# Kernel tuning notes

Hardware: AMD Instinct MI355X
Metric: run time of the kernel (lower is better)

The kernel has to match this reference:

```python
import jax, jax.numpy as jnp
import numpy as np

EPS = 1e-06


def setup_inputs() -> dict:
    key = jax.random.key(0)
    k1, k2, k3 = jax.random.split(key, 3)
    B, L, S, C = 128, 512, 512, 64
    q = jax.random.normal(k1, (B, L, C), dtype=jnp.float32)
    k = jax.random.normal(k2, (B, S, C), dtype=jnp.float32)
    labels = jax.random.randint(k3, (B, L, S), 0, 2, dtype=jnp.int64)
    return {"q": q, "k": k, "labels": labels}


def reference(q, k, labels):
    # sim: [B, L, S], mapped to (0, 1) via (1 + cos-like sim) / 2
    sim = (1.0 + jnp.einsum('blc,bsc->bls', q, k)) * 0.5

    # column-wise stats (over L) -> [B, S]; torch.std uses ddof=1 (unbiased)
    col = (jnp.max(sim, axis=1) - jnp.mean(sim, axis=1)) / jnp.std(sim, axis=1, ddof=1)
    sharp1 = jax.nn.softmax(col, axis=-1)  # [B, S]

    # row-wise stats (over S) -> [B, L]
    row = (jnp.max(sim, axis=2) - jnp.mean(sim, axis=2)) / jnp.std(sim, axis=2, ddof=1)
    sharp2 = jax.nn.softmax(row, axis=-1)  # [B, L]

    simc = jnp.clip(sim, EPS, 1.0 - EPS)
    nll = -jnp.log(simc)                    # [B, L, S]
    nll_neg = -jnp.log(1.0 - simc)          # [B, L, S]

    pos = (labels == 1).astype(sim.dtype)
    neg = (labels == 0).astype(sim.dtype)

    # masked sums per sample, weighted by sharpness (broadcast over rows/cols)
    loss1 = jnp.sum(nll * sharp1[:, None, :] * pos, axis=(1, 2))  # [B]
    loss2 = jnp.sum(nll * sharp2[:, :, None] * pos, axis=(1, 2))  # [B]
    loss3 = jnp.sum(nll_neg * neg, axis=(1, 2)) / jnp.sum(neg, axis=(1, 2))  # [B]

    losses = (loss1 + loss2) * 0.5 + loss3
    return (sharp1, jnp.mean(losses))
```

## Files before the change

kernel.cpp:

```cpp
#include <hip/hip_runtime.h>

#define EPSF 1e-6f

typedef _Float16 half8 __attribute__((ext_vector_type(8)));
typedef float f32x4 __attribute__((ext_vector_type(4)));

constexpr int B = 128, L = 512, S = 512, C = 64;
constexpr int TILE_R = 64;
constexpr int TILES  = L / TILE_R;
constexpr int CHUNK  = 64;
constexpr int NCHUNK = S / CHUNK;
constexpr int HALVES = 2;
constexpr int CPB    = NCHUNK / HALVES;

constexpr size_t WS_COLMAX = 0;
constexpr size_t WS_COLSUM = WS_COLMAX + (size_t)B * TILES * S;
constexpr size_t WS_COLSSQ = WS_COLSUM + (size_t)B * TILES * S;
constexpr size_t WS_COLP1  = WS_COLSSQ + (size_t)B * TILES * S;
constexpr size_t WS_ROWMAX = WS_COLP1  + (size_t)B * TILES * S;
constexpr size_t WS_ROWSUM = WS_ROWMAX + (size_t)B * L * HALVES;
constexpr size_t WS_ROWSSQ = WS_ROWSUM + (size_t)B * L * HALVES;
constexpr size_t WS_ROWP2  = WS_ROWSSQ + (size_t)B * L * HALVES;
constexpr size_t WS_NEGS   = WS_ROWP2  + (size_t)B * L * HALVES;
constexpr size_t WS_NEGC   = WS_NEGS   + (size_t)B * TILES * HALVES;
constexpr size_t WS_QF     = WS_NEGC   + (size_t)B * TILES * HALVES;
constexpr size_t WS_KF     = WS_QF     + (size_t)B * TILES * 4096;
constexpr size_t WS_LP     = WS_KF     + (size_t)B * NCHUNK * 4096;

constexpr int PACK_ROWS   = 4;
constexpr int CONV_BLOCKS = B * (TILES + NCHUNK);
constexpr int PACK_BLOCKS = B * L / PACK_ROWS;

__device__ inline void loadTile(const float* __restrict__ g, float4 v[4], int t)
{
    const float* src = g + (t >> 2) * 64 + (t & 3) * 16;
    v[0] = *(const float4*)(src);
    v[1] = *(const float4*)(src + 4);
    v[2] = *(const float4*)(src + 8);
    v[3] = *(const float4*)(src + 12);
}

__device__ inline void fragStore(const float4 v4[4], half8* dhi, half8* dlo, int t)
{
    const int row = t >> 2, c0 = (t & 3) * 16;
    const float v[16] = {v4[0].x, v4[0].y, v4[0].z, v4[0].w, v4[1].x, v4[1].y, v4[1].z, v4[1].w,
                         v4[2].x, v4[2].y, v4[2].z, v4[2].w, v4[3].x, v4[3].y, v4[3].z, v4[3].w};
#pragma unroll
    for (int o = 0; o < 2; ++o) {
        const int cb     = c0 + o * 8;
        const int idx    = (row >> 4) * 2 + (cb >> 5);
        const int lane_s = (((cb >> 3) & 3) << 4) + (row & 15);
        half8 h, l;
#pragma unroll
        for (int j = 0; j < 8; ++j) {
            float f = v[o * 8 + j];
            _Float16 hi = (_Float16)f;
            h[j] = hi;
            l[j] = (_Float16)(f - (float)hi);
        }
        dhi[idx * 64 + lane_s] = h;
        dlo[idx * 64 + lane_s] = l;
    }
}

__global__ __launch_bounds__(256)
void convert_kernel(const float* __restrict__ q, const float* __restrict__ kmat,
                    const int* __restrict__ labels, float* __restrict__ ws)
{
    const int bidx = blockIdx.x;
    const int tid  = threadIdx.x;

    if (bidx < CONV_BLOCKS) {
        const int b    = bidx >> 4;
        const int t16  = bidx & 15;
        const bool isq = (t16 < TILES);
        const int tile = isq ? t16 : t16 - TILES;

        const float* src = isq ? (q    + ((size_t)b * L + (size_t)tile * TILE_R) * C)
                               : (kmat + ((size_t)b * S + (size_t)tile * CHUNK)  * C);
        half8* base = (half8*)(ws + (isq ? WS_QF : WS_KF)) + (size_t)(b * TILES + tile) * 1024;

        float4 v[4];
        loadTile(src, v, tid);
        fragStore(v, base, base + 512, tid);
    } else {
        const int pb   = bidx - CONV_BLOCKS;
        const int b    = pb / (L / PACK_ROWS);
        const int rg   = pb % (L / PACK_ROWS);
        const int wave = tid >> 6, lane = tid & 63;
        const size_t row = (size_t)b * L + rg * PACK_ROWS + wave;
        const int* src = labels + row * S;
        unsigned long long* dst = (unsigned long long*)(ws + WS_LP) + row * 8;
        int v[8];
#pragma unroll
        for (int w = 0; w < 8; ++w)
            v[w] = __builtin_nontemporal_load(&src[w * 64 + lane]);
#pragma unroll
        for (int w = 0; w < 8; ++w) {
            unsigned long long m = __ballot(v[w] == 1);
            if (lane == 0) dst[w] = m;
        }
    }
}

__device__ inline void gl16(const void* g, void* l)
{
    __builtin_amdgcn_global_load_lds((const __attribute__((address_space(1))) void*)g,
                                     (__attribute__((address_space(3))) void*)l, 16, 0, 0);
}

__global__ __launch_bounds__(256) __attribute__((amdgpu_waves_per_eu(3, 8)))
void pass1_kernel(float* __restrict__ ws)
{
    __shared__ half8 kbuf[2][1024];
    __shared__ float4 colred4[4][CPB][CHUNK];
    __shared__ float nred[4][2];

    const int bidx = blockIdx.x;
    const int b    = bidx / (TILES * HALVES);
    const int rem  = bidx % (TILES * HALVES);
    const int tile = rem >> 1;
    const int half = rem & 1;
    const int chbase = half * CPB;
    const int tid  = threadIdx.x;
    const int lane = tid & 63;
    const int wave = tid >> 6;
    const int l15  = lane & 15;
    const int quad = lane >> 4;
    const int rowbase = tile * TILE_R;

    float* colmax_p = ws + WS_COLMAX;
    float* colsum_p = ws + WS_COLSUM;
    float* colssq_p = ws + WS_COLSSQ;
    float* colp1_p  = ws + WS_COLP1;
    float* rowmax_p = ws + WS_ROWMAX;
    float* rowsum_p = ws + WS_ROWSUM;
    float* rowssq_p = ws + WS_ROWSSQ;
    float* rowp2_p  = ws + WS_ROWP2;
    float* negs_p   = ws + WS_NEGS;
    float* negc_p   = ws + WS_NEGC;

    const half8* qf  = (const half8*)(ws + WS_QF) + (size_t)(b * TILES + tile) * 1024;
    const half8* kf0 = (const half8*)(ws + WS_KF) + (size_t)b * NCHUNK * 1024;
    const unsigned long long* lp =
        (const unsigned long long*)(ws + WS_LP) + ((size_t)b * L + rowbase) * 8;

    auto stage = [&](int ch, int bi) {
#pragma unroll
        for (int i = 0; i < 4; ++i)
            gl16(kf0 + (size_t)ch * 1024 + i * 256 + tid,
                 &kbuf[bi][i * 256 + (tid & 192)]);
    };

    stage(chbase, 0);

    half8 ah0 = qf[(wave * 2 + 0) * 64 + lane];
    half8 ah1 = qf[(wave * 2 + 1) * 64 + lane];
    half8 al0 = qf[512 + (wave * 2 + 0) * 64 + lane];
    half8 al1 = qf[512 + (wave * 2 + 1) * 64 + lane];

    float rmax[4], rsum[4], rssq[4], rp2[4];
#pragma unroll
    for (int i = 0; i < 4; ++i) { rmax[i] = -3.4e38f; rsum[i] = 0.f; rssq[i] = 0.f; rp2[i] = 0.f; }
    float negsum = 0.f;
    int   possum = 0;

    __syncthreads();

    for (int c4 = 0; c4 < CPB; ++c4) {
        const int ch = chbase + c4;
        if (c4 + 1 < CPB) stage(ch + 1, (c4 + 1) & 1);
        const half8* kb = kbuf[c4 & 1];

        unsigned long long lw[4];
#pragma unroll
        for (int r = 0; r < 4; ++r)
            lw[r] = lp[(size_t)(wave * 16 + quad * 4 + r) * 8 + ch];

        f32x4 acc[4];
#pragma unroll
        for (int ct = 0; ct < 4; ++ct) {
            half8 bh0 = kb[(ct * 2 + 0) * 64 + lane];
            half8 bh1 = kb[(ct * 2 + 1) * 64 + lane];
            half8 bl0 = kb[512 + (ct * 2 + 0) * 64 + lane];
            half8 bl1 = kb[512 + (ct * 2 + 1) * 64 + lane];
            f32x4 a = {0.f, 0.f, 0.f, 0.f};
            a = __builtin_amdgcn_mfma_f32_16x16x32_f16(ah0, bh0, a, 0, 0, 0);
            a = __builtin_amdgcn_mfma_f32_16x16x32_f16(ah0, bl0, a, 0, 0, 0);
            a = __builtin_amdgcn_mfma_f32_16x16x32_f16(al0, bh0, a, 0, 0, 0);
            a = __builtin_amdgcn_mfma_f32_16x16x32_f16(ah1, bh1, a, 0, 0, 0);
            a = __builtin_amdgcn_mfma_f32_16x16x32_f16(ah1, bl1, a, 0, 0, 0);
            a = __builtin_amdgcn_mfma_f32_16x16x32_f16(al1, bh1, a, 0, 0, 0);
            acc[ct] = a;
        }

#pragma unroll
        for (int ct = 0; ct < 4; ++ct) {
            float cmax = -3.4e38f, csum = 0.f, cssq = 0.f, cp1 = 0.f;
#pragma unroll
            for (int r = 0; r < 4; ++r) {
                int lab = (int)((lw[r] >> (ct * 16 + l15)) & 1ull);
                float sim = fmaf(0.5f, acc[ct][r], 0.5f);
                rmax[r] = fmaxf(rmax[r], sim);
                rsum[r] += sim;
                rssq[r] = fmaf(sim, sim, rssq[r]);
                cmax = fmaxf(cmax, sim);
                csum += sim;
                cssq = fmaf(sim, sim, cssq);
                float sc  = fminf(fmaxf(sim, EPSF), 1.f - EPSF);
                bool  isp = (lab == 1);
                float pos = isp ? 1.f : 0.f;
                float t   = isp ? sc : (1.f - sc);
                float nl  = -__logf(t);
                float pn  = pos * nl;
                rp2[r] += pn;
                cp1 += pn;
                negsum += nl - pn;
                possum += lab;
            }
#pragma unroll
            for (int m = 16; m <= 32; m <<= 1) {
                cmax = fmaxf(cmax, __shfl_xor(cmax, m, 64));
                csum += __shfl_xor(csum, m, 64);
                cssq += __shfl_xor(cssq, m, 64);
                cp1  += __shfl_xor(cp1,  m, 64);
            }
            if (lane < 16)
                colred4[wave][c4][ct * 16 + l15] = make_float4(cmax, csum, cssq, cp1);
        }

        __syncthreads();
    }

    {
        const int cc  = tid >> 6;
        const int col = tid & 63;
        float4 v = colred4[0][cc][col];
        float m0 = v.x, s1 = v.y, s2 = v.z, pp = v.w;
#pragma unroll
        for (int w = 1; w < 4; ++w) {
            float4 u = colred4[w][cc][col];
            m0 = fmaxf(m0, u.x); s1 += u.y; s2 += u.z; pp += u.w;
        }
        size_t idx = ((size_t)b * TILES + tile) * S + (chbase + cc) * CHUNK + col;
        colmax_p[idx] = m0; colsum_p[idx] = s1; colssq_p[idx] = s2; colp1_p[idx] = pp;
    }

#pragma unroll
    for (int r = 0; r < 4; ++r) {
#pragma unroll
        for (int m = 1; m <= 8; m <<= 1) {
            rmax[r] = fmaxf(rmax[r], __shfl_xor(rmax[r], m, 64));
            rsum[r] += __shfl_xor(rsum[r], m, 64);
            rssq[r] += __shfl_xor(rssq[r], m, 64);
            rp2[r]  += __shfl_xor(rp2[r],  m, 64);
        }
    }
    if (l15 == 0) {
#pragma unroll
        for (int r = 0; r < 4; ++r) {
            size_t idx = ((size_t)b * L + rowbase + wave * 16 + quad * 4 + r) * HALVES + half;
            rowmax_p[idx] = rmax[r]; rowsum_p[idx] = rsum[r];
            rowssq_p[idx] = rssq[r]; rowp2_p[idx]  = rp2[r];
        }
    }

    float negcnt = (float)(16 * CPB - possum);
#pragma unroll
    for (int m = 1; m <= 32; m <<= 1) {
        negsum += __shfl_xor(negsum, m, 64);
        negcnt += __shfl_xor(negcnt, m, 64);
    }
    if (lane == 0) { nred[wave][0] = negsum; nred[wave][1] = negcnt; }
    __syncthreads();
    if (tid == 0) {
        float ns = 0.f, nc = 0.f;
        for (int w = 0; w < 4; ++w) { ns += nred[w][0]; nc += nred[w][1]; }
        negs_p[bidx] = ns; negc_p[bidx] = nc;
    }
}

template <bool MAX>
__device__ inline float bred(float v, float* red)
{
#pragma unroll
    for (int m = 1; m <= 32; m <<= 1) {
        float o = __shfl_xor(v, m, 64);
        v = MAX ? fmaxf(v, o) : (v + o);
    }
    const int wave = threadIdx.x >> 6;
    const int lane = threadIdx.x & 63;
    if (lane == 0) red[wave] = v;
    __syncthreads();
    if (threadIdx.x == 0) {
        float r = red[0];
        for (int w = 1; w < 8; ++w) r = MAX ? fmaxf(r, red[w]) : (r + red[w]);
        red[8] = r;
    }
    __syncthreads();
    float out = red[8];
    __syncthreads();
    return out;
}

__global__ __launch_bounds__(512)
void pass2_kernel(const float* __restrict__ ws, float* __restrict__ out)
{
    __shared__ float red[9];
    const int b = blockIdx.x;
    const int s = threadIdx.x;

    if (blockIdx.y == 0) {
        const float* colmax_p = ws + WS_COLMAX;
        const float* colsum_p = ws + WS_COLSUM;
        const float* colssq_p = ws + WS_COLSSQ;
        const float* colp1_p  = ws + WS_COLP1;

        float m = -3.4e38f, sm = 0.f, sq = 0.f, p1 = 0.f;
#pragma unroll
        for (int t = 0; t < TILES; ++t) {
            size_t idx = ((size_t)b * TILES + t) * S + s;
            m = fmaxf(m, colmax_p[idx]);
            sm += colsum_p[idx];
            sq += colssq_p[idx];
            p1 += colp1_p[idx];
        }
        float mean  = sm * (1.f / L);
        float var   = (sq - sm * sm * (1.f / L)) * (1.f / (L - 1));
        float score = (m - mean) / sqrtf(var);

        float gmax = bred<true>(score, red);
        float e    = __expf(score - gmax);
        float esum = bred<false>(e, red);
        float sharp1 = e / esum;
        out[(size_t)b * S + s] = sharp1;
        float loss1 = bred<false>(sharp1 * p1, red);
        if (s == 0) atomicAdd(out + (size_t)B * S, loss1 * (0.5f / B));
    } else {
        const float* rowmax_p = ws + WS_ROWMAX;
        const float* rowsum_p = ws + WS_ROWSUM;
        const float* rowssq_p = ws + WS_ROWSSQ;
        const float* rowp2_p  = ws + WS_ROWP2;
        const float* negs_p   = ws + WS_NEGS;
        const float* negc_p   = ws + WS_NEGC;

        size_t ridx = ((size_t)b * L + s) * HALVES;
        float m2 = rowmax_p[ridx], sm2 = rowsum_p[ridx];
        float sq2 = rowssq_p[ridx], p2 = rowp2_p[ridx];
#pragma unroll
        for (int h = 1; h < HALVES; ++h) {
            m2 = fmaxf(m2, rowmax_p[ridx + h]);
            sm2 += rowsum_p[ridx + h];
            sq2 += rowssq_p[ridx + h];
            p2  += rowp2_p[ridx + h];
        }
        float mean2  = sm2 * (1.f / S);
        float var2   = (sq2 - sm2 * sm2 * (1.f / S)) * (1.f / (S - 1));
        float score2 = (m2 - mean2) / sqrtf(var2);

        float gmax2 = bred<true>(score2, red);
        float e2    = __expf(score2 - gmax2);
        float esum2 = bred<false>(e2, red);
        float loss2 = bred<false>((e2 / esum2) * p2, red);

        if (s == 0) {
            float ns = 0.f, nc = 0.f;
            for (int t = 0; t < TILES * HALVES; ++t) {
                ns += negs_p[b * TILES * HALVES + t];
                nc += negc_p[b * TILES * HALVES + t];
            }
            atomicAdd(out + (size_t)B * S, (0.5f * loss2 + ns / nc) * (1.f / B));
        }
    }
}

extern "C" void kernel_launch(void* const* d_in, const int* in_sizes, int n_in,
                              void* d_out, int out_size, void* d_ws, size_t ws_size,
                              hipStream_t stream)
{
    const float* q      = (const float*)d_in[0];
    const float* k      = (const float*)d_in[1];
    const int*   labels = (const int*)d_in[2];
    float* out = (float*)d_out;
    float* ws  = (float*)d_ws;

    hipMemsetAsync((char*)d_out + (size_t)B * S * sizeof(float), 0, sizeof(float), stream);

    convert_kernel<<<dim3(CONV_BLOCKS + PACK_BLOCKS), dim3(256), 0, stream>>>(q, k, labels, ws);
    pass1_kernel<<<dim3(B * TILES * HALVES), dim3(256), 0, stream>>>(ws);
    pass2_kernel<<<dim3(B, 2), dim3(512), 0, stream>>>(ws, out);
}
```

Baseline: 271.4 us.

## Drop column-half split, triple-buffer K chunks and stage labels in LDS

Each pass1 block now covers all 8 K chunks of its row tile instead of half, which removes the two-way split of row partials and halves the block count. K fragments are triple-buffered with explicit vmcnt waits and a single barrier per chunk, and each chunk's column reduction is written out one iteration later so it overlaps with compute. The label bitmasks for the tile are loaded once into LDS rather than read from global memory every chunk. The hipMemset is replaced by a store inside convert_kernel. The trade-offs are fewer blocks (1024) to fill the GPU, a lower waves-per-EU hint, and hand-written waitcnt counts that depend on exactly how many loads are outstanding.

```diff
diff --git a/kernel.cpp b/kernel.cpp
--- a/kernel.cpp
+++ b/kernel.cpp
@@ -10,20 +10,18 @@
 constexpr int TILES  = L / TILE_R;
 constexpr int CHUNK  = 64;
 constexpr int NCHUNK = S / CHUNK;
-constexpr int HALVES = 2;
-constexpr int CPB    = NCHUNK / HALVES;
 
 constexpr size_t WS_COLMAX = 0;
 constexpr size_t WS_COLSUM = WS_COLMAX + (size_t)B * TILES * S;
 constexpr size_t WS_COLSSQ = WS_COLSUM + (size_t)B * TILES * S;
 constexpr size_t WS_COLP1  = WS_COLSSQ + (size_t)B * TILES * S;
 constexpr size_t WS_ROWMAX = WS_COLP1  + (size_t)B * TILES * S;
-constexpr size_t WS_ROWSUM = WS_ROWMAX + (size_t)B * L * HALVES;
-constexpr size_t WS_ROWSSQ = WS_ROWSUM + (size_t)B * L * HALVES;
-constexpr size_t WS_ROWP2  = WS_ROWSSQ + (size_t)B * L * HALVES;
-constexpr size_t WS_NEGS   = WS_ROWP2  + (size_t)B * L * HALVES;
-constexpr size_t WS_NEGC   = WS_NEGS   + (size_t)B * TILES * HALVES;
-constexpr size_t WS_QF     = WS_NEGC   + (size_t)B * TILES * HALVES;
+constexpr size_t WS_ROWSUM = WS_ROWMAX + (size_t)B * L;
+constexpr size_t WS_ROWSSQ = WS_ROWSUM + (size_t)B * L;
+constexpr size_t WS_ROWP2  = WS_ROWSSQ + (size_t)B * L;
+constexpr size_t WS_NEGS   = WS_ROWP2  + (size_t)B * L;
+constexpr size_t WS_NEGC   = WS_NEGS   + (size_t)B * TILES;
+constexpr size_t WS_QF     = WS_NEGC   + (size_t)B * TILES;
 constexpr size_t WS_KF     = WS_QF     + (size_t)B * TILES * 4096;
 constexpr size_t WS_LP     = WS_KF     + (size_t)B * NCHUNK * 4096;
 
@@ -65,10 +63,12 @@
 
 __global__ __launch_bounds__(256)
 void convert_kernel(const float* __restrict__ q, const float* __restrict__ kmat,
-                    const int* __restrict__ labels, float* __restrict__ ws)
+                    const int* __restrict__ labels, float* __restrict__ ws,
+                    float* __restrict__ out)
 {
     const int bidx = blockIdx.x;
     const int tid  = threadIdx.x;
+    if (bidx == 0 && tid == 0) out[(size_t)B * S] = 0.f;
 
     if (bidx < CONV_BLOCKS) {
         const int b    = bidx >> 4;
@@ -109,19 +109,17 @@
                                      (__attribute__((address_space(3))) void*)l, 16, 0, 0);
 }
 
-__global__ __launch_bounds__(256) __attribute__((amdgpu_waves_per_eu(3, 8)))
+__global__ __launch_bounds__(256) __attribute__((amdgpu_waves_per_eu(2, 8)))
 void pass1_kernel(float* __restrict__ ws)
 {
-    __shared__ half8 kbuf[2][1024];
-    __shared__ float4 colred4[4][CPB][CHUNK];
+    __shared__ half8 kbuf[3][1024];
+    __shared__ float4 colred[2][4][CHUNK];
+    __shared__ unsigned long long labL[64 * 10];
     __shared__ float nred[4][2];
 
     const int bidx = blockIdx.x;
-    const int b    = bidx / (TILES * HALVES);
-    const int rem  = bidx % (TILES * HALVES);
-    const int tile = rem >> 1;
-    const int half = rem & 1;
-    const int chbase = half * CPB;
+    const int b    = bidx / TILES;
+    const int tile = bidx % TILES;
     const int tid  = threadIdx.x;
     const int lane = tid & 63;
     const int wave = tid >> 6;
@@ -152,7 +150,14 @@
                  &kbuf[bi][i * 256 + (tid & 192)]);
     };
 
-    stage(chbase, 0);
+    stage(0, 0);
+    stage(1, 1);
+
+    {
+        const ulonglong2 lv = *(const ulonglong2*)(lp + tid * 2);
+        const int row = tid >> 2, w = (tid & 3) * 2;
+        *(ulonglong2*)&labL[row * 10 + w] = lv;
+    }
 
     half8 ah0 = qf[(wave * 2 + 0) * 64 + lane];
     half8 ah1 = qf[(wave * 2 + 1) * 64 + lane];
@@ -165,17 +170,34 @@
     float negsum = 0.f;
     int   possum = 0;
 
-    __syncthreads();
-
-    for (int c4 = 0; c4 < CPB; ++c4) {
-        const int ch = chbase + c4;
-        if (c4 + 1 < CPB) stage(ch + 1, (c4 + 1) & 1);
-        const half8* kb = kbuf[c4 & 1];
+    for (int c4 = 0; c4 < NCHUNK; ++c4) {
+        if (c4 < 2 || c4 == NCHUNK - 1)
+            asm volatile("s_waitcnt vmcnt(4) lgkmcnt(0)" ::: "memory");
+        else
+            asm volatile("s_waitcnt vmcnt(8) lgkmcnt(0)" ::: "memory");
+        __builtin_amdgcn_s_barrier();
+        asm volatile("" ::: "memory");
+
+        if (c4 > 0 && lane < 16) {
+            const int col  = wave * 16 + l15;
+            const int slot = (c4 - 1) & 1;
+            float4 v = colred[slot][0][col];
+            float m0 = v.x, s1 = v.y, s2 = v.z, pp = v.w;
+#pragma unroll
+            for (int w = 1; w < 4; ++w) {
+                float4 u = colred[slot][w][col];
+                m0 = fmaxf(m0, u.x); s1 += u.y; s2 += u.z; pp += u.w;
+            }
+            size_t idx = ((size_t)b * TILES + tile) * S + (size_t)(c4 - 1) * CHUNK + col;
+            colmax_p[idx] = m0; colsum_p[idx] = s1; colssq_p[idx] = s2; colp1_p[idx] = pp;
+        }
+
+        const half8* kb = kbuf[c4 % 3];
 
         unsigned long long lw[4];
 #pragma unroll
         for (int r = 0; r < 4; ++r)
-            lw[r] = lp[(size_t)(wave * 16 + quad * 4 + r) * 8 + ch];
+            lw[r] = labL[(wave * 16 + quad * 4 + r) * 10 + c4];
 
         f32x4 acc[4];
 #pragma unroll
@@ -226,23 +248,24 @@
                 cp1  += __shfl_xor(cp1,  m, 64);
             }
             if (lane < 16)
-                colred4[wave][c4][ct * 16 + l15] = make_float4(cmax, csum, cssq, cp1);
-        }
-
-        __syncthreads();
-    }
-
-    {
-        const int cc  = tid >> 6;
-        const int col = tid & 63;
-        float4 v = colred4[0][cc][col];
+                colred[c4 & 1][wave][ct * 16 + l15] = make_float4(cmax, csum, cssq, cp1);
+        }
+
+        if (c4 + 2 < NCHUNK) stage(c4 + 2, (c4 + 2) % 3);
+    }
+
+    __syncthreads();
+    if (lane < 16) {
+        const int col  = wave * 16 + l15;
+        const int slot = (NCHUNK - 1) & 1;
+        float4 v = colred[slot][0][col];
         float m0 = v.x, s1 = v.y, s2 = v.z, pp = v.w;
 #pragma unroll
         for (int w = 1; w < 4; ++w) {
-            float4 u = colred4[w][cc][col];
+            float4 u = colred[slot][w][col];
             m0 = fmaxf(m0, u.x); s1 += u.y; s2 += u.z; pp += u.w;
         }
-        size_t idx = ((size_t)b * TILES + tile) * S + (chbase + cc) * CHUNK + col;
+        size_t idx = ((size_t)b * TILES + tile) * S + (size_t)(NCHUNK - 1) * CHUNK + col;
         colmax_p[idx] = m0; colsum_p[idx] = s1; colssq_p[idx] = s2; colp1_p[idx] = pp;
     }
 
@@ -259,13 +282,13 @@
     if (l15 == 0) {
 #pragma unroll
         for (int r = 0; r < 4; ++r) {
-            size_t idx = ((size_t)b * L + rowbase + wave * 16 + quad * 4 + r) * HALVES + half;
+            size_t idx = (size_t)b * L + rowbase + wave * 16 + quad * 4 + r;
             rowmax_p[idx] = rmax[r]; rowsum_p[idx] = rsum[r];
             rowssq_p[idx] = rssq[r]; rowp2_p[idx]  = rp2[r];
         }
     }
 
-    float negcnt = (float)(16 * CPB - possum);
+    float negcnt = (float)(16 * NCHUNK - possum);
 #pragma unroll
     for (int m = 1; m <= 32; m <<= 1) {
         negsum += __shfl_xor(negsum, m, 64);
@@ -344,16 +367,12 @@
         const float* negs_p   = ws + WS_NEGS;
         const float* negc_p   = ws + WS_NEGC;
 
-        size_t ridx = ((size_t)b * L + s) * HALVES;
-        float m2 = rowmax_p[ridx], sm2 = rowsum_p[ridx];
-        float sq2 = rowssq_p[ridx], p2 = rowp2_p[ridx];
-#pragma unroll
-        for (int h = 1; h < HALVES; ++h) {
-            m2 = fmaxf(m2, rowmax_p[ridx + h]);
-            sm2 += rowsum_p[ridx + h];
-            sq2 += rowssq_p[ridx + h];
-            p2  += rowp2_p[ridx + h];
-        }
+        size_t ridx = (size_t)b * L + s;
+        float m2  = rowmax_p[ridx];
+        float sm2 = rowsum_p[ridx];
+        float sq2 = rowssq_p[ridx];
+        float p2  = rowp2_p[ridx];
+
         float mean2  = sm2 * (1.f / S);
         float var2   = (sq2 - sm2 * sm2 * (1.f / S)) * (1.f / (S - 1));
         float score2 = (m2 - mean2) / sqrtf(var2);
@@ -365,9 +384,9 @@
 
         if (s == 0) {
             float ns = 0.f, nc = 0.f;
-            for (int t = 0; t < TILES * HALVES; ++t) {
-                ns += negs_p[b * TILES * HALVES + t];
-                nc += negc_p[b * TILES * HALVES + t];
+            for (int t = 0; t < TILES; ++t) {
+                ns += negs_p[b * TILES + t];
+                nc += negc_p[b * TILES + t];
             }
             atomicAdd(out + (size_t)B * S, (0.5f * loss2 + ns / nc) * (1.f / B));
         }
@@ -384,9 +403,7 @@
     float* out = (float*)d_out;
     float* ws  = (float*)d_ws;
 
-    hipMemsetAsync((char*)d_out + (size_t)B * S * sizeof(float), 0, sizeof(float), stream);
-
-    convert_kernel<<<dim3(CONV_BLOCKS + PACK_BLOCKS), dim3(256), 0, stream>>>(q, k, labels, ws);
-    pass1_kernel<<<dim3(B * TILES * HALVES), dim3(256), 0, stream>>>(ws);
+    convert_kernel<<<dim3(CONV_BLOCKS + PACK_BLOCKS), dim3(256), 0, stream>>>(q, k, labels, ws, out);
+    pass1_kernel<<<dim3(B * TILES), dim3(256), 0, stream>>>(ws);
     pass2_kernel<<<dim3(B, 2), dim3(512), 0, stream>>>(ws, out);
 }
```

Measured after the change: 274.6 us. About the same (+1.2%).
